# Kernel optimization log

Measured on AMD Instinct MI355X. Metric: run time of the kernel, lower is better.

The kernel has to match this reference:

```python
import jax, jax.numpy as jnp
import numpy as np

D_K = 64

def setup_inputs() -> dict:
    key = jax.random.key(0)
    k1, k2, k3, k4 = jax.random.split(key, 4)
    hidden_states = jax.random.normal(k1, (2, 16, 128, 16, 16), dtype=jnp.float32)
    # nn.Linear(hidden, d, bias=False); stored as [in, out] for x @ W
    w_q = jax.random.normal(k2, (128, 64), dtype=jnp.float32) * 0.05
    w_k = jax.random.normal(k3, (128, 64), dtype=jnp.float32) * 0.05
    w_v = jax.random.normal(k4, (128, 64), dtype=jnp.float32) * 0.05
    return {"hidden_states": hidden_states, "w_q": w_q, "w_k": w_k, "w_v": w_v}

def reference(hidden_states, w_q, w_k, w_v):
    # (B, T, C, H, W) -> (B, T, H, W, C) -> (N, C)
    x = jnp.transpose(hidden_states, (0, 1, 3, 4, 2))
    x = x.reshape(-1, x.shape[-1])                      # [N, C], N = B*T*H*W
    q = x @ w_q                                          # [N, d_k]
    k = x @ w_k                                          # [N, d_k]
    v = x @ w_v                                          # [N, d_v]
    scores = (q @ k.T) / jnp.sqrt(jnp.asarray(D_K, x.dtype))  # [N, N]
    attn = jax.nn.softmax(scores, axis=1)                # softmax over dim=1
    out = attn @ v                                       # [N, d_v]
    return out
```

## Files before the change

kernel.cpp:

```cpp
#include <hip/hip_runtime.h>
#include <hip/hip_bf16.h>

typedef float f32x4 __attribute__((ext_vector_type(4)));
typedef short bf16x8 __attribute__((ext_vector_type(8)));
typedef short bf16x4 __attribute__((ext_vector_type(4)));

#define MFMA32 __builtin_amdgcn_mfma_f32_16x16x32_bf16

#if __has_builtin(__builtin_amdgcn_mfma_f32_16x16x16bf16_1k)
#define HAVE_MFMA16 1
#else
#define HAVE_MFMA16 0
#endif

__device__ __forceinline__ unsigned short f2bf(float f) {
  union { float f; unsigned u; } v; v.f = f;
  unsigned u = v.u;
  u += 0x7FFFu + ((u >> 16) & 1u);
  return (unsigned short)(u >> 16);
}

__device__ __forceinline__ bf16x4 pack4_bf16(float a, float b, float c, float d) {
  union { bf16x4 v; __hip_bfloat162 h[2]; } u;
  u.h[0] = __float22bfloat162_rn(make_float2(a, b));
  u.h[1] = __float22bfloat162_rn(make_float2(c, d));
  return u.v;
}

__device__ __forceinline__ f32x4 pv_mfma(bf16x4 av, bf16x4 pf, f32x4 acc) {
#if HAVE_MFMA16
  return __builtin_amdgcn_mfma_f32_16x16x16bf16_1k(av, pf, acc, 0, 0, 0);
#else
  bf16x8 a8 = {av[0], av[1], av[2], av[3], 0, 0, 0, 0};
  bf16x8 b8 = {pf[0], pf[1], pf[2], pf[3], 0, 0, 0, 0};
  return MFMA32(a8, b8, acc, 0, 0, 0);
#endif
}

__global__ __launch_bounds__(256) void qkv_kernel(
    const float* __restrict__ hs,
    const float* __restrict__ wq, const float* __restrict__ wk,
    const float* __restrict__ wv,
    unsigned short* __restrict__ qb, unsigned short* __restrict__ kpack,
    unsigned short* __restrict__ vpack)
{
  __shared__ __align__(16) float Wl[128 * 64];
  __shared__ float xs[32 * 129];
  const int t = threadIdx.x;
  const int mat = blockIdx.y;
  const float* __restrict__ W = (mat == 0) ? wq : (mat == 1) ? wk : wv;
  #pragma unroll
  for (int i = 0; i < 8; ++i) {
    *(f32x4*)(Wl + i * 1024 + t * 4) = *(const f32x4*)(W + i * 1024 + t * 4);
  }
  const int n0 = blockIdx.x * 32;
  const int bt = n0 >> 8;
  const int sp0 = n0 & 255;
  {
    const float* __restrict__ src = hs + (size_t)bt * 32768 + sp0;
    const int s = t & 31, cb = t >> 5;
    #pragma unroll
    for (int i = 0; i < 16; ++i) {
      const int c = i * 8 + cb;
      xs[s * 129 + c] = src[c * 256 + s];
    }
  }
  __syncthreads();
  const int s = t & 31, g = t >> 5;
  float acc[8];
  #pragma unroll
  for (int j = 0; j < 8; ++j) acc[j] = 0.f;
  #pragma unroll 4
  for (int c = 0; c < 128; ++c) {
    const float xv = xs[s * 129 + c];
    const f32x4 w0 = *(const f32x4*)(Wl + c * 64 + g * 8);
    const f32x4 w1 = *(const f32x4*)(Wl + c * 64 + g * 8 + 4);
    acc[0] += xv * w0[0]; acc[1] += xv * w0[1];
    acc[2] += xv * w0[2]; acc[3] += xv * w0[3];
    acc[4] += xv * w1[0]; acc[5] += xv * w1[1];
    acc[6] += xv * w1[2]; acc[7] += xv * w1[3];
  }
  const int n = n0 + s;
  const float SCALE = 1.4426950408889634f / 8.0f;
  if (mat == 0) {
    #pragma unroll
    for (int j = 0; j < 8; ++j) qb[n * 64 + g * 8 + j] = f2bf(acc[j] * SCALE);
  } else if (mat == 1) {
    const int kvb = n >> 4, low16 = n & 15;
    const int h = g >> 2, quadk = g & 3;
    unsigned short* dst = kpack + ((size_t)(kvb * 2 + h) * 64 + quadk * 16 + low16) * 8;
    #pragma unroll
    for (int j = 0; j < 8; ++j) dst[j] = f2bf(acc[j]);
  } else {
    const int kvb = n >> 4, quadv = (n >> 2) & 3, ii = n & 3;
    #pragma unroll
    for (int j = 0; j < 8; ++j) {
      const int d = g * 8 + j, dt = d >> 4, lowd = d & 15;
      vpack[((size_t)(kvb * 4 + dt) * 64 + quadv * 16 + lowd) * 4 + ii] = f2bf(acc[j]);
    }
  }
}

__global__ __launch_bounds__(256, 3) void flash_kernel(
    const unsigned short* __restrict__ qb,
    const unsigned short* __restrict__ kpack,
    const unsigned short* __restrict__ vpack,
    float* __restrict__ opart, float* __restrict__ lpart, int kvlen)
{
  const int t = threadIdx.x;
  const int w = t >> 6, lane = t & 63;
  const int quad = lane >> 4, low = lane & 15;
  const int bid = blockIdx.x;
  const int q0 = (bid & 31) * 256 + w * 64;
  const int g = bid >> 5;
  const int kvb0 = (g * kvlen) >> 4;
  const int nIter = kvlen >> 4;

  bf16x8 bq[4][2];
  #pragma unroll
  for (int qt = 0; qt < 4; ++qt)
    #pragma unroll
    for (int h = 0; h < 2; ++h)
      bq[qt][h] = *(const bf16x8*)(qb + (q0 + qt * 16 + low) * 64 + h * 32 + quad * 8);

  f32x4 O[4][4];
  float lac[4] = {0.f, 0.f, 0.f, 0.f};
  #pragma unroll
  for (int qt = 0; qt < 4; ++qt)
    #pragma unroll
    for (int dt = 0; dt < 4; ++dt) O[qt][dt] = (f32x4){0.f, 0.f, 0.f, 0.f};

  const unsigned short* kp = kpack + (size_t)kvb0 * 1024 + lane * 8;
  const unsigned short* vp = vpack + (size_t)kvb0 * 1024 + lane * 4;

  bf16x8 k0[2], k1[2], k2[2];
  bf16x4 v0[4], v1[4], v2[4];
  k0[0] = *(const bf16x8*)(kp);
  k0[1] = *(const bf16x8*)(kp + 512);
  #pragma unroll
  for (int dt = 0; dt < 4; ++dt) v0[dt] = *(const bf16x4*)(vp + dt * 256);
  const int i1 = (nIter > 1) ? 1 : 0;
  k1[0] = *(const bf16x8*)(kp + (size_t)i1 * 1024);
  k1[1] = *(const bf16x8*)(kp + (size_t)i1 * 1024 + 512);
  #pragma unroll
  for (int dt = 0; dt < 4; ++dt)
    v1[dt] = *(const bf16x4*)(vp + (size_t)i1 * 1024 + dt * 256);

  #pragma unroll 3
  for (int it = 0; it < nIter; ++it) {
    const int nx = (it + 2 < nIter) ? it + 2 : nIter - 1;
    k2[0] = *(const bf16x8*)(kp + (size_t)nx * 1024);
    k2[1] = *(const bf16x8*)(kp + (size_t)nx * 1024 + 512);
    #pragma unroll
    for (int dt = 0; dt < 4; ++dt)
      v2[dt] = *(const bf16x4*)(vp + (size_t)nx * 1024 + dt * 256);

    #pragma unroll
    for (int qt = 0; qt < 4; ++qt) {
      f32x4 S = {0.f, 0.f, 0.f, 0.f};
      S = MFMA32(k0[0], bq[qt][0], S, 0, 0, 0);
      S = MFMA32(k0[1], bq[qt][1], S, 0, 0, 0);
      const float p0 = __builtin_amdgcn_exp2f(S[0]);
      const float p1 = __builtin_amdgcn_exp2f(S[1]);
      const float p2 = __builtin_amdgcn_exp2f(S[2]);
      const float p3 = __builtin_amdgcn_exp2f(S[3]);
      lac[qt] += (p0 + p1) + (p2 + p3);
      const bf16x4 pf = pack4_bf16(p0, p1, p2, p3);
      #pragma unroll
      for (int dt = 0; dt < 4; ++dt)
        O[qt][dt] = pv_mfma(v0[dt], pf, O[qt][dt]);
    }
    k0[0] = k1[0]; k0[1] = k1[1];
    k1[0] = k2[0]; k1[1] = k2[1];
    #pragma unroll
    for (int dt = 0; dt < 4; ++dt) { v0[dt] = v1[dt]; v1[dt] = v2[dt]; }
  }

  #pragma unroll
  for (int qt = 0; qt < 4; ++qt) {
    const size_t qrow = (size_t)g * 8192 + q0 + qt * 16;
    #pragma unroll
    for (int dt = 0; dt < 4; ++dt)
      *(f32x4*)(opart + (qrow + low) * 64 + dt * 16 + quad * 4) = O[qt][dt];
    float l = lac[qt];
    l += __shfl_xor(l, 16);
    l += __shfl_xor(l, 32);
    if (quad == 0) lpart[qrow + low] = l;
  }
}

__global__ __launch_bounds__(256) void reduce_kernel(
    const float* __restrict__ opart, const float* __restrict__ lpart,
    float* __restrict__ out, int G)
{
  const int idx = blockIdx.x * 256 + threadIdx.x;
  const int q = idx >> 4;
  const int d4 = (idx & 15) * 4;
  float den = 0.f;
  f32x4 num = {0.f, 0.f, 0.f, 0.f};
  for (int g = 0; g < G; ++g) {
    den += lpart[g * 8192 + q];
    const f32x4 o = *(const f32x4*)(opart + ((size_t)g * 8192 + q) * 64 + d4);
    num[0] += o[0]; num[1] += o[1]; num[2] += o[2]; num[3] += o[3];
  }
  const float r = 1.0f / den;
  f32x4 res = {num[0] * r, num[1] * r, num[2] * r, num[3] * r};
  *(f32x4*)(out + (size_t)q * 64 + d4) = res;
}

extern "C" void kernel_launch(void* const* d_in, const int* in_sizes, int n_in,
                              void* d_out, int out_size, void* d_ws, size_t ws_size,
                              hipStream_t stream) {
  const float* hs = (const float*)d_in[0];
  const float* wq = (const float*)d_in[1];
  const float* wk = (const float*)d_in[2];
  const float* wv = (const float*)d_in[3];
  float* out = (float*)d_out;
  char* ws = (char*)d_ws;

  unsigned short* qb    = (unsigned short*)ws;
  unsigned short* kpack = (unsigned short*)(ws + (1 << 20));
  unsigned short* vpack = (unsigned short*)(ws + (2 << 20));

  int G = 32;
  {
    const size_t per_g = (size_t)8192 * 64 * 4 + (size_t)8192 * 4;
    while (G > 1 && ws_size < (size_t)(3 << 20) + (size_t)G * per_g) G >>= 1;
  }
  float* opart = (float*)(ws + (3 << 20));
  float* lpart = (float*)(ws + (3 << 20) + (size_t)G * 8192 * 64 * 4);

  qkv_kernel<<<dim3(256, 3, 1), 256, 0, stream>>>(hs, wq, wk, wv, qb, kpack, vpack);
  flash_kernel<<<32 * G, 256, 0, stream>>>(qb, kpack, vpack, opart, lpart, 8192 / G);
  reduce_kernel<<<512, 256, 0, stream>>>(opart, lpart, out, G);
}
```

Before: 117.8 us.

## Stage K/V chunks in LDS via direct global-to-LDS loads and use full-K 32-wide MFMAs

The flash kernel now double-buffers 128-key chunks of K and V in shared memory with global_load_lds and block-level barriers, so the four waves share one staged copy instead of each streaming K/V from global into registers. K and V are repacked for 32-key blocks so the P·V product uses the full 16x16x32 bf16 MFMA rather than the 16-wide variant. The row sum is computed with an extra MFMA against a ones vector in place of the shuffle reduction. The split count G drops to 16 and occupancy is hinted at 2 blocks per CU, trading parallelism and added LDS pressure and barriers for fewer global loads and fewer MFMA issues.

```diff
diff --git a/kernel.cpp b/kernel.cpp
--- a/kernel.cpp
+++ b/kernel.cpp
@@ -3,15 +3,8 @@
 
 typedef float f32x4 __attribute__((ext_vector_type(4)));
 typedef short bf16x8 __attribute__((ext_vector_type(8)));
-typedef short bf16x4 __attribute__((ext_vector_type(4)));
 
 #define MFMA32 __builtin_amdgcn_mfma_f32_16x16x32_bf16
-
-#if __has_builtin(__builtin_amdgcn_mfma_f32_16x16x16bf16_1k)
-#define HAVE_MFMA16 1
-#else
-#define HAVE_MFMA16 0
-#endif
 
 __device__ __forceinline__ unsigned short f2bf(float f) {
   union { float f; unsigned u; } v; v.f = f;
@@ -20,20 +13,24 @@
   return (unsigned short)(u >> 16);
 }
 
-__device__ __forceinline__ bf16x4 pack4_bf16(float a, float b, float c, float d) {
-  union { bf16x4 v; __hip_bfloat162 h[2]; } u;
-  u.h[0] = __float22bfloat162_rn(make_float2(a, b));
-  u.h[1] = __float22bfloat162_rn(make_float2(c, d));
+__device__ __forceinline__ bf16x8 pack8_bf16(float a, float b, float c, float d,
+                                             float e, float f, float g, float h) {
+  union { bf16x8 v; __hip_bfloat162 p[4]; } u;
+  u.p[0] = __float22bfloat162_rn(make_float2(a, b));
+  u.p[1] = __float22bfloat162_rn(make_float2(c, d));
+  u.p[2] = __float22bfloat162_rn(make_float2(e, f));
+  u.p[3] = __float22bfloat162_rn(make_float2(g, h));
   return u.v;
 }
 
-__device__ __forceinline__ f32x4 pv_mfma(bf16x4 av, bf16x4 pf, f32x4 acc) {
-#if HAVE_MFMA16
-  return __builtin_amdgcn_mfma_f32_16x16x16bf16_1k(av, pf, acc, 0, 0, 0);
+__device__ __forceinline__ void stage16(const unsigned short* gbase,
+                                        unsigned short* lbase, int lane) {
+#if __has_builtin(__builtin_amdgcn_global_load_lds)
+  __builtin_amdgcn_global_load_lds(
+      (const __attribute__((address_space(1))) void*)(gbase + lane * 8),
+      (__attribute__((address_space(3))) void*)lbase, 16, 0, 0);
 #else
-  bf16x8 a8 = {av[0], av[1], av[2], av[3], 0, 0, 0, 0};
-  bf16x8 b8 = {pf[0], pf[1], pf[2], pf[3], 0, 0, 0, 0};
-  return MFMA32(a8, b8, acc, 0, 0, 0);
+  *(bf16x8*)(lbase + lane * 8) = *(const bf16x8*)(gbase + lane * 8);
 #endif
 }
 
@@ -86,35 +83,42 @@
     #pragma unroll
     for (int j = 0; j < 8; ++j) qb[n * 64 + g * 8 + j] = f2bf(acc[j] * SCALE);
   } else if (mat == 1) {
-    const int kvb = n >> 4, low16 = n & 15;
+    const int kvb32 = n >> 5, kvl = n & 31;
+    const int ti = (kvl >> 2) & 1;
+    const int lowk = ((kvl >> 3) << 2) | (kvl & 3);
     const int h = g >> 2, quadk = g & 3;
-    unsigned short* dst = kpack + ((size_t)(kvb * 2 + h) * 64 + quadk * 16 + low16) * 8;
+    unsigned short* dst =
+        kpack + (((size_t)(kvb32 * 2 + ti) * 2 + h) * 64 + quadk * 16 + lowk) * 8;
     #pragma unroll
     for (int j = 0; j < 8; ++j) dst[j] = f2bf(acc[j]);
   } else {
-    const int kvb = n >> 4, quadv = (n >> 2) & 3, ii = n & 3;
-    #pragma unroll
-    for (int j = 0; j < 8; ++j) {
-      const int d = g * 8 + j, dt = d >> 4, lowd = d & 15;
-      vpack[((size_t)(kvb * 4 + dt) * 64 + quadv * 16 + lowd) * 4 + ii] = f2bf(acc[j]);
-    }
-  }
-}
-
-__global__ __launch_bounds__(256, 3) void flash_kernel(
+    const int kvb32 = n >> 5, kvl = n & 31;
+    const int quadv = kvl >> 3, jj = kvl & 7;
+    #pragma unroll
+    for (int jw = 0; jw < 8; ++jw) {
+      const int d = g * 8 + jw, dt = d >> 4, lowd = d & 15;
+      vpack[(((size_t)kvb32 * 4 + dt) * 64 + quadv * 16 + lowd) * 8 + jj] =
+          f2bf(acc[jw]);
+    }
+  }
+}
+
+__global__ __launch_bounds__(256, 2) void flash_kernel(
     const unsigned short* __restrict__ qb,
     const unsigned short* __restrict__ kpack,
     const unsigned short* __restrict__ vpack,
     float* __restrict__ opart, float* __restrict__ lpart, int kvlen)
 {
+  __shared__ __align__(16) unsigned short Kl[2][4][2048];
+  __shared__ __align__(16) unsigned short Vl[2][4][2048];
   const int t = threadIdx.x;
   const int w = t >> 6, lane = t & 63;
   const int quad = lane >> 4, low = lane & 15;
   const int bid = blockIdx.x;
   const int q0 = (bid & 31) * 256 + w * 64;
   const int g = bid >> 5;
-  const int kvb0 = (g * kvlen) >> 4;
-  const int nIter = kvlen >> 4;
+  const int kvb32_0 = (g * kvlen) >> 5;
+  const int nch = kvlen >> 7;
 
   bf16x8 bq[4][2];
   #pragma unroll
@@ -124,56 +128,63 @@
       bq[qt][h] = *(const bf16x8*)(qb + (q0 + qt * 16 + low) * 64 + h * 32 + quad * 8);
 
   f32x4 O[4][4];
-  float lac[4] = {0.f, 0.f, 0.f, 0.f};
-  #pragma unroll
-  for (int qt = 0; qt < 4; ++qt)
+  f32x4 O4[4];
+  #pragma unroll
+  for (int qt = 0; qt < 4; ++qt) {
     #pragma unroll
     for (int dt = 0; dt < 4; ++dt) O[qt][dt] = (f32x4){0.f, 0.f, 0.f, 0.f};
-
-  const unsigned short* kp = kpack + (size_t)kvb0 * 1024 + lane * 8;
-  const unsigned short* vp = vpack + (size_t)kvb0 * 1024 + lane * 4;
-
-  bf16x8 k0[2], k1[2], k2[2];
-  bf16x4 v0[4], v1[4], v2[4];
-  k0[0] = *(const bf16x8*)(kp);
-  k0[1] = *(const bf16x8*)(kp + 512);
-  #pragma unroll
-  for (int dt = 0; dt < 4; ++dt) v0[dt] = *(const bf16x4*)(vp + dt * 256);
-  const int i1 = (nIter > 1) ? 1 : 0;
-  k1[0] = *(const bf16x8*)(kp + (size_t)i1 * 1024);
-  k1[1] = *(const bf16x8*)(kp + (size_t)i1 * 1024 + 512);
-  #pragma unroll
-  for (int dt = 0; dt < 4; ++dt)
-    v1[dt] = *(const bf16x4*)(vp + (size_t)i1 * 1024 + dt * 256);
-
-  #pragma unroll 3
-  for (int it = 0; it < nIter; ++it) {
-    const int nx = (it + 2 < nIter) ? it + 2 : nIter - 1;
-    k2[0] = *(const bf16x8*)(kp + (size_t)nx * 1024);
-    k2[1] = *(const bf16x8*)(kp + (size_t)nx * 1024 + 512);
-    #pragma unroll
-    for (int dt = 0; dt < 4; ++dt)
-      v2[dt] = *(const bf16x4*)(vp + (size_t)nx * 1024 + dt * 256);
-
-    #pragma unroll
-    for (int qt = 0; qt < 4; ++qt) {
-      f32x4 S = {0.f, 0.f, 0.f, 0.f};
-      S = MFMA32(k0[0], bq[qt][0], S, 0, 0, 0);
-      S = MFMA32(k0[1], bq[qt][1], S, 0, 0, 0);
-      const float p0 = __builtin_amdgcn_exp2f(S[0]);
-      const float p1 = __builtin_amdgcn_exp2f(S[1]);
-      const float p2 = __builtin_amdgcn_exp2f(S[2]);
-      const float p3 = __builtin_amdgcn_exp2f(S[3]);
-      lac[qt] += (p0 + p1) + (p2 + p3);
-      const bf16x4 pf = pack4_bf16(p0, p1, p2, p3);
+    O4[qt] = (f32x4){0.f, 0.f, 0.f, 0.f};
+  }
+  const bf16x8 ones = {16256, 16256, 16256, 16256, 16256, 16256, 16256, 16256};
+
+  #define STAGE_CHUNK(b, c)                                                   \
+    {                                                                         \
+      const size_t kb = (size_t)(kvb32_0 + (c) * 4 + w) * 2048;               \
+      _Pragma("unroll")                                                       \
+      for (int r = 0; r < 4; ++r) {                                           \
+        stage16(kpack + kb + r * 512, &Kl[b][w][r * 512], lane);              \
+        stage16(vpack + kb + r * 512, &Vl[b][w][r * 512], lane);              \
+      }                                                                       \
+    }
+
+  STAGE_CHUNK(0, 0)
+  __syncthreads();
+
+  for (int c = 0; c < nch; ++c) {
+    const int b = c & 1;
+    if (c + 1 < nch) STAGE_CHUNK(b ^ 1, c + 1)
+    #pragma unroll
+    for (int j = 0; j < 4; ++j) {
+      bf16x8 kf[4], vf[4];
       #pragma unroll
-      for (int dt = 0; dt < 4; ++dt)
-        O[qt][dt] = pv_mfma(v0[dt], pf, O[qt][dt]);
-    }
-    k0[0] = k1[0]; k0[1] = k1[1];
-    k1[0] = k2[0]; k1[1] = k2[1];
-    #pragma unroll
-    for (int dt = 0; dt < 4; ++dt) { v0[dt] = v1[dt]; v1[dt] = v2[dt]; }
+      for (int f = 0; f < 4; ++f)
+        kf[f] = *(const bf16x8*)&Kl[b][j][f * 512 + lane * 8];
+      #pragma unroll
+      for (int f = 0; f < 4; ++f)
+        vf[f] = *(const bf16x8*)&Vl[b][j][f * 512 + lane * 8];
+      #pragma unroll
+      for (int qt = 0; qt < 4; ++qt) {
+        f32x4 SA = {0.f, 0.f, 0.f, 0.f}, SB = {0.f, 0.f, 0.f, 0.f};
+        SA = MFMA32(kf[0], bq[qt][0], SA, 0, 0, 0);
+        SA = MFMA32(kf[1], bq[qt][1], SA, 0, 0, 0);
+        SB = MFMA32(kf[2], bq[qt][0], SB, 0, 0, 0);
+        SB = MFMA32(kf[3], bq[qt][1], SB, 0, 0, 0);
+        const float pa0 = __builtin_amdgcn_exp2f(SA[0]);
+        const float pa1 = __builtin_amdgcn_exp2f(SA[1]);
+        const float pa2 = __builtin_amdgcn_exp2f(SA[2]);
+        const float pa3 = __builtin_amdgcn_exp2f(SA[3]);
+        const float pb0 = __builtin_amdgcn_exp2f(SB[0]);
+        const float pb1 = __builtin_amdgcn_exp2f(SB[1]);
+        const float pb2 = __builtin_amdgcn_exp2f(SB[2]);
+        const float pb3 = __builtin_amdgcn_exp2f(SB[3]);
+        const bf16x8 pf = pack8_bf16(pa0, pa1, pa2, pa3, pb0, pb1, pb2, pb3);
+        #pragma unroll
+        for (int dt = 0; dt < 4; ++dt)
+          O[qt][dt] = MFMA32(vf[dt], pf, O[qt][dt], 0, 0, 0);
+        O4[qt] = MFMA32(ones, pf, O4[qt], 0, 0, 0);
+      }
+    }
+    __syncthreads();
   }
 
   #pragma unroll
@@ -182,10 +193,7 @@
     #pragma unroll
     for (int dt = 0; dt < 4; ++dt)
       *(f32x4*)(opart + (qrow + low) * 64 + dt * 16 + quad * 4) = O[qt][dt];
-    float l = lac[qt];
-    l += __shfl_xor(l, 16);
-    l += __shfl_xor(l, 32);
-    if (quad == 0) lpart[qrow + low] = l;
+    if (quad == 0) lpart[qrow + low] = O4[qt][0];
   }
 }
 
@@ -222,7 +230,7 @@
   unsigned short* kpack = (unsigned short*)(ws + (1 << 20));
   unsigned short* vpack = (unsigned short*)(ws + (2 << 20));
 
-  int G = 32;
+  int G = 16;
   {
     const size_t per_g = (size_t)8192 * 64 * 4 + (size_t)8192 * 4;
     while (G > 1 && ws_size < (size_t)(3 << 20) + (size_t)G * per_g) G >>= 1;
```

After: 98.28 us. 1.2x faster.
